# Optimization experiments

Hardware: AMD Instinct MI355X
Metric: run time of the kernel (lower is better)

## Reference

```python
import jax, jax.numpy as jnp
import numpy as np

MU_P = 0.15
MASK_ID = 103
VOCAB = 30522


def setup_inputs() -> dict:
    key = jax.random.key(0)
    k1, k2 = jax.random.split(key)
    B, C, S = 1024, 4, 2048
    # first half = per-token sampling weights, second half = shared_tokens (unused by the math)
    my_attention_mask = jax.random.uniform(k1, (B, C, 2 * S), dtype=jnp.float32)
    attention_mask = jnp.ones((B, C, S), dtype=jnp.int32)  # tokenizer attention mask
    input_ids = jax.random.randint(k2, (B, C, S), 0, VOCAB, dtype=jnp.int32)
    return {"my_attention_mask": my_attention_mask,
            "attention_mask": attention_mask,
            "input_ids": input_ids}


def reference(my_attention_mask, attention_mask, input_ids):
    """Weighted sampling WITHOUT replacement per (batch, choice) row via Gumbel-top-k.

    Original loops over (k, j), draws num_to_mask = floor(sum(tok_mask) * N(mu_p, sigma))
    indices from the nonzero weights in my_attention_mask[..., :S] (prob ~ weight),
    masks those token positions in input_ids and emits the indicator mask.
    Gumbel-top-k: keys = log(w) + Gumbel noise; the top-num_to_mask keys are a
    weighted sample without replacement from w. Zero-weight positions get -inf keys.
    """
    B, C, S = input_ids.shape
    w = my_attention_mask[..., :S]  # [B, C, S] sampling weights

    key = jax.random.key(42)
    kg, kn = jax.random.split(key)
    sigma = min(0.05, MU_P / 4.0)
    frac = MU_P + sigma * jax.random.normal(kn, (B, C), dtype=jnp.float32)
    num_to_mask = jnp.floor(
        attention_mask.sum(axis=-1).astype(jnp.float32) * frac
    ).astype(jnp.int32)  # [B, C]

    log_w = jnp.where(w > 0, jnp.log(jnp.maximum(w, 1e-30)), -jnp.inf)
    keys = log_w + jax.random.gumbel(kg, w.shape, dtype=jnp.float32)  # [B, C, S]

    # rank[i] = position of i in descending key order (double argsort)
    order = jnp.argsort(-keys, axis=-1)
    rank = jnp.argsort(order, axis=-1)
    new_attention_mask = (rank < num_to_mask[..., None]).astype(jnp.int32)  # [B, C, S]

    new_input_ids = jnp.where(new_attention_mask == 1, MASK_ID, input_ids)
    discriminator_labels = -new_attention_mask
    return new_input_ids, new_attention_mask, discriminator_labels
```

## Files before the change

### kernel.cpp

```cpp
#include <hip/hip_runtime.h>
#include <stdint.h>
#include <math.h>

#define SLEN 2048
#define EPT 8
#define NTHREADS 256
#define TOKENS_PER_OUT 8388608

__host__ __device__ __forceinline__ void tf2x32(uint32_t k0, uint32_t k1,
                                                uint32_t x0, uint32_t x1,
                                                uint32_t &o0, uint32_t &o1) {
  uint32_t ks2 = 0x1BD11BDAu ^ k0 ^ k1;
  x0 += k0; x1 += k1;
#define TFR(r) { x0 += x1; x1 = (x1 << (r)) | (x1 >> (32 - (r))); x1 ^= x0; }
  TFR(13) TFR(15) TFR(26) TFR(6)
  x0 += k1;  x1 += ks2 + 1u;
  TFR(17) TFR(29) TFR(16) TFR(24)
  x0 += ks2; x1 += k0 + 2u;
  TFR(13) TFR(15) TFR(26) TFR(6)
  x0 += k0;  x1 += k1 + 3u;
  TFR(17) TFR(29) TFR(16) TFR(24)
  x0 += k1;  x1 += ks2 + 4u;
  TFR(13) TFR(15) TFR(26) TFR(6)
  x0 += ks2; x1 += k0 + 5u;
#undef TFR
  o0 = x0; o1 = x1;
}

__device__ __forceinline__ void tf4_bits(uint32_t k0, uint32_t k1,
                                         uint32_t cbase, uint32_t bits[4]) {
  const uint32_t ks2 = 0x1BD11BDAu ^ k0 ^ k1;
  uint32_t x0[4], x1[4];
#pragma unroll
  for (int i = 0; i < 4; ++i) { x0[i] = k0; x1[i] = (cbase + (uint32_t)i) + k1; }
#define TFR4(r)                                                         \
  _Pragma("unroll")                                                     \
  for (int i = 0; i < 4; ++i) {                                         \
    x0[i] += x1[i];                                                     \
    x1[i] = (x1[i] << (r)) | (x1[i] >> (32 - (r)));                     \
    x1[i] ^= x0[i];                                                     \
  }
#define INJ4(a, b)                                                      \
  _Pragma("unroll")                                                     \
  for (int i = 0; i < 4; ++i) { x0[i] += (a); x1[i] += (b); }
  TFR4(13) TFR4(15) TFR4(26) TFR4(6)
  INJ4(k1, ks2 + 1u)
  TFR4(17) TFR4(29) TFR4(16) TFR4(24)
  INJ4(ks2, k0 + 2u)
  TFR4(13) TFR4(15) TFR4(26) TFR4(6)
  INJ4(k0, k1 + 3u)
  TFR4(17) TFR4(29) TFR4(16) TFR4(24)
  INJ4(k1, ks2 + 4u)
  TFR4(13) TFR4(15) TFR4(26) TFR4(6)
  INJ4(ks2, k0 + 5u)
#undef TFR4
#undef INJ4
#pragma unroll
  for (int i = 0; i < 4; ++i) bits[i] = x0[i] ^ x1[i];
}

__device__ __forceinline__ float u01_from_bits(uint32_t bits) {
  return __uint_as_float((bits >> 9) | 0x3F800000u) - 1.0f;
}

__device__ __forceinline__ void log4_cr(const float x[4], float out[4]) {
#pragma clang fp contract(off)
  double m[4]; int e[4];
#pragma unroll
  for (int i = 0; i < 4; ++i) {
    long long b = __double_as_longlong((double)x[i]);
    e[i] = (int)(b >> 52) - 1023;
    m[i] = __longlong_as_double((b & 0x000FFFFFFFFFFFFFLL) | 0x3FF0000000000000LL);
  }
#pragma unroll
  for (int i = 0; i < 4; ++i) {
    bool c = m[i] > 1.4142135623730951;
    m[i] = c ? 0.5 * m[i] : m[i];
    e[i] += c ? 1 : 0;
  }
  double mp1[4], y[4];
#pragma unroll
  for (int i = 0; i < 4; ++i) mp1[i] = m[i] + 1.0;
#pragma unroll
  for (int i = 0; i < 4; ++i) y[i] = __builtin_amdgcn_rcp(mp1[i]);
#pragma unroll
  for (int i = 0; i < 4; ++i) y[i] = fma(fma(-mp1[i], y[i], 1.0), y[i], y[i]);
  double r[4], t[4], p[4];
#pragma unroll
  for (int i = 0; i < 4; ++i) r[i] = (m[i] - 1.0) * y[i];
#pragma unroll
  for (int i = 0; i < 4; ++i) t[i] = r[i] * r[i];
#pragma unroll
  for (int i = 0; i < 4; ++i) p[i] = fma(0.07692307692307693, t[i], 0.09090909090909091);
#pragma unroll
  for (int i = 0; i < 4; ++i) p[i] = fma(p[i], t[i], 0.1111111111111111);
#pragma unroll
  for (int i = 0; i < 4; ++i) p[i] = fma(p[i], t[i], 0.14285714285714285);
#pragma unroll
  for (int i = 0; i < 4; ++i) p[i] = fma(p[i], t[i], 0.2);
#pragma unroll
  for (int i = 0; i < 4; ++i) p[i] = fma(p[i], t[i], 0.3333333333333333);
#pragma unroll
  for (int i = 0; i < 4; ++i) p[i] = fma(p[i], t[i], 1.0);
#pragma unroll
  for (int i = 0; i < 4; ++i)
    out[i] = (float)fma((double)e[i], 0.6931471805599453, 2.0 * (r[i] * p[i]));
}

__device__ __forceinline__ float log_cr(float x) {
  float in[4] = {x, x, x, x}, o[4];
  log4_cr(in, o);
  return o[0];
}

__device__ float erfinv_xla(float x) {
#pragma clang fp contract(off)
  float x2  = x * x;
  float nx2 = -x2;
  float l1p;
  if (fabsf(nx2) < 1e-4f) {
    l1p = (-0.5f * nx2 + 1.0f) * nx2;
  } else {
    l1p = log_cr(1.0f + nx2);
  }
  float w = -l1p;
  float p;
  if (w < 5.0f) {
    float ww = w - 2.5f;
    p = 2.81022636e-08f;
    p = p * ww + 3.43273939e-07f;
    p = p * ww + -3.5233877e-06f;
    p = p * ww + -4.39150654e-06f;
    p = p * ww + 0.00021858087f;
    p = p * ww + -0.00125372503f;
    p = p * ww + -0.00417768164f;
    p = p * ww + 0.246640727f;
    p = p * ww + 1.50140941f;
  } else {
    float ww = sqrtf(w) - 3.0f;
    p = -0.000200214257f;
    p = p * ww + 0.000100950558f;
    p = p * ww + 0.00134934322f;
    p = p * ww + -0.00367342844f;
    p = p * ww + 0.00573950773f;
    p = p * ww + -0.0076224613f;
    p = p * ww + 0.00943887047f;
    p = p * ww + 1.00167406f;
    p = p * ww + 2.83297682f;
  }
  return p * x;
}

__global__ __launch_bounds__(NTHREADS, 6)
void gumbel_topk_mask(const float* __restrict__ wfull,
                      const int*   __restrict__ attn,
                      const int*   __restrict__ ids,
                      int* __restrict__ out,
                      uint32_t kg0, uint32_t kg1, uint32_t kn0, uint32_t kn1) {
#pragma clang fp contract(off)
  const int row  = blockIdx.x;
  const int t    = threadIdx.x;
  const int lane = t & 63;
  const int wid  = t >> 6;

  __shared__ __align__(16) uint32_t hist[2][256];
  __shared__ uint32_t wsum[4];
  __shared__ uint32_t prefix_s;
  __shared__ uint32_t remaining_s;
  __shared__ int      done_s;

  const size_t rbase = (size_t)row * SLEN;
  const size_t wbase = (size_t)row * (2 * SLEN);
  const int    base  = t * EPT;

  hist[0][t] = 0u;
  hist[1][t] = 0u;

  const float4* wv4 = (const float4*)(wfull + wbase + base);
  float4 w0 = wv4[0], w1 = wv4[1];
  const int4* av4 = (const int4*)(attn + rbase + base);
  int4 a0 = av4[0], a1 = av4[1];
  const int4* iv4 = (const int4*)(ids + rbase + base);
  int4 i0 = iv4[0], i1 = iv4[1];
  int psum = a0.x + a0.y + a0.z + a0.w + a1.x + a1.y + a1.z + a1.w;

  float wl[EPT] = {w0.x, w0.y, w0.z, w0.w, w1.x, w1.y, w1.z, w1.w};
  uint32_t mloc[EPT];
#pragma unroll
  for (int g = 0; g < 2; ++g) {
    uint32_t bits[4];
    tf4_bits(kg0, kg1, (uint32_t)(rbase + base + 4 * g), bits);
    float uu[4];
#pragma unroll
    for (int j = 0; j < 4; ++j) {
      float f = u01_from_bits(bits[j]);
      uu[j] = fmaxf(1.17549435e-38f, f * 1.0f + 1.17549435e-38f);
    }
    float l1[4];
    log4_cr(uu, l1);
    float wm[4];
#pragma unroll
    for (int j = 0; j < 4; ++j) wm[j] = fmaxf(wl[4 * g + j], 1e-30f);
    float lw[4];
    log4_cr(wm, lw);
    float nl1[4];
#pragma unroll
    for (int j = 0; j < 4; ++j) nl1[j] = -l1[j];
    float l2[4];
    log4_cr(nl1, l2);
#pragma unroll
    for (int j = 0; j < 4; ++j) {
      float key = (wl[4 * g + j] > 0.0f) ? (lw[j] + (-l2[j])) : -__builtin_inff();
      uint32_t kb = __float_as_uint(key);
      uint32_t mv = (kb & 0x80000000u) ? ~kb : (kb | 0x80000000u);
      mloc[4 * g + j] = mv;
    }
  }

#pragma unroll
  for (int off = 32; off; off >>= 1) psum += __shfl_down(psum, off, 64);
  if (lane == 0) wsum[wid] = (uint32_t)psum;
  if (t == 0) { prefix_s = 0u; done_s = 0; }
  __syncthreads();

#pragma unroll
  for (int e = 0; e < EPT; ++e) atomicAdd(&hist[0][mloc[e] >> 24], 1u);

  int cur = 0;
  for (int p = 3; p >= 0; --p) {
    __syncthreads();
    if (t < 64) {
      uint32_t need = 0u;
      if (p == 3) {
        int asum = (int)(wsum[0] + wsum[1] + wsum[2] + wsum[3]);
        uint32_t o0, o1;
        tf2x32(kn0, kn1, 0u, (uint32_t)row, o0, o1);
        float f   = u01_from_bits(o0 ^ o1);
        float lo  = __uint_as_float(0xBF7FFFFFu);
        float u2  = fmaxf(lo, f * 2.0f + lo);
        float z   = erfinv_xla(u2);
        float nrm = 1.4142135623730951f * z;
        float frac = 0.15f + 0.0375f * nrm;
        int kk = (int)floorf((float)asum * frac);
        if (kk <= 0)         { if (t == 0) { prefix_s = 0xFFFFFFFFu; remaining_s = 0u;   done_s = 1; } }
        else if (kk >= SLEN) { if (t == 0) { prefix_s = 0u;          remaining_s = SLEN; done_s = 1; } }
        else need = (uint32_t)kk;
      } else {
        need = remaining_s;
      }
      if (need) {
        uint4 hq = ((const uint4*)hist[cur])[t];
        uint32_t gs  = hq.x + hq.y + hq.z + hq.w;
        uint32_t sfx = gs;
#pragma unroll
        for (int off = 1; off < 64; off <<= 1) {
          uint32_t n = __shfl_down(sfx, off, 64);
          if (t + off < 64) sfx += n;
        }
        uint32_t Gex = sfx - gs;
        uint32_t S3 = Gex;
        uint32_t S2 = S3 + hq.w;
        uint32_t S1 = S2 + hq.z;
        uint32_t S0 = S1 + hq.y;
        uint32_t hh[4] = {hq.x, hq.y, hq.z, hq.w};
        uint32_t SS[4] = {S0, S1, S2, S3};
#pragma unroll
        for (int i = 0; i < 4; ++i) {
          if (hh[i] && SS[i] < need && need <= SS[i] + hh[i]) {
            prefix_s |= ((uint32_t)(4 * t + i)) << (8 * p);
            uint32_t rem = need - SS[i];
            remaining_s = rem;
            if (rem == hh[i]) done_s = 1;
          }
        }
      }
    } else {
      int idx = t - 64;
      hist[cur ^ 1][idx] = 0u;
      if (idx < 64) hist[cur ^ 1][idx + 192] = 0u;
    }
    __syncthreads();
    if (done_s) break;
    if (p > 0) {
      uint32_t pref = prefix_s;
      int sh = 8 * p;
#pragma unroll
      for (int e = 0; e < EPT; ++e) {
        uint32_t m = mloc[e];
        if ((m >> sh) == (pref >> sh))
          atomicAdd(&hist[cur ^ 1][(m >> (sh - 8)) & 255u], 1u);
      }
    }
    cur ^= 1;
  }
  uint32_t T = prefix_s;
  uint32_t r = remaining_s;

  int local_eq = 0;
#pragma unroll
  for (int e = 0; e < EPT; ++e) local_eq += (mloc[e] == T) ? 1 : 0;
  uint32_t v = (uint32_t)local_eq;
#pragma unroll
  for (int off = 1; off < 64; off <<= 1) {
    uint32_t n = __shfl_up(v, off, 64);
    if (lane >= off) v += n;
  }
  if (lane == 63) wsum[wid] = v;
  __syncthreads();
  uint32_t add = 0;
  for (int i = 0; i < wid; ++i) add += wsum[i];
  uint32_t excl = add + v - (uint32_t)local_eq;

  int idv[EPT] = {i0.x, i0.y, i0.z, i0.w, i1.x, i1.y, i1.z, i1.w};
  int oid[EPT], omk[EPT], olb[EPT];
#pragma unroll
  for (int e = 0; e < EPT; ++e) {
    uint32_t m = mloc[e];
    bool eq  = (m == T);
    bool msk = (m > T) || (eq && (excl < r));
    excl += eq ? 1u : 0u;
    oid[e] = msk ? 103 : idv[e];
    omk[e] = msk ? 1 : 0;
    olb[e] = msk ? -1 : 0;
  }
  int4* po = (int4*)(out + rbase + base);
  po[0] = make_int4(oid[0], oid[1], oid[2], oid[3]);
  po[1] = make_int4(oid[4], oid[5], oid[6], oid[7]);
  int4* pm = (int4*)(out + TOKENS_PER_OUT + rbase + base);
  pm[0] = make_int4(omk[0], omk[1], omk[2], omk[3]);
  pm[1] = make_int4(omk[4], omk[5], omk[6], omk[7]);
  int4* pl = (int4*)(out + 2 * TOKENS_PER_OUT + rbase + base);
  pl[0] = make_int4(olb[0], olb[1], olb[2], olb[3]);
  pl[1] = make_int4(olb[4], olb[5], olb[6], olb[7]);
}

extern "C" void kernel_launch(void* const* d_in, const int* in_sizes, int n_in,
                              void* d_out, int out_size, void* d_ws, size_t ws_size,
                              hipStream_t stream) {
  (void)n_in; (void)d_ws; (void)ws_size; (void)out_size;
  const float* wfull = (const float*)d_in[0];
  const int*   attn  = (const int*)d_in[1];
  const int*   ids   = (const int*)d_in[2];
  int* out = (int*)d_out;

  uint32_t kg0, kg1, kn0, kn1, o0, o1;
  tf2x32(0u, 42u, 0u, 0u, o0, o1); kg0 = o0; kg1 = o1;
  tf2x32(0u, 42u, 0u, 1u, o0, o1); kn0 = o0; kn1 = o1;

  int rows = in_sizes[1] / SLEN;
  hipLaunchKernelGGL(gumbel_topk_mask, dim3(rows), dim3(NTHREADS), 0, stream,
                     wfull, attn, ids, out, kg0, kg1, kn0, kn1);
}
```

Baseline: 207.5 us.

## Batch logs 8-wide with sched barriers and integer-based mantissa extraction

Widens the double-precision log routine from 4 to 8 lanes and puts scheduling barriers between each polynomial stage, so independent FP64 ops interleave and hide latency. Mantissa/exponent extraction now uses 32-bit integer ops on the float bits instead of a float-to-double conversion. The scalar log also loses its wasted 4-wide evaluation. Launch bounds drop from 6 to 5 blocks per CU to allow more registers, which risks lower occupancy and latency hiding.

```diff
diff --git a/kernel.cpp b/kernel.cpp
--- a/kernel.cpp
+++ b/kernel.cpp
@@ -39,7 +39,8 @@
     x0[i] += x1[i];                                                     \
     x1[i] = (x1[i] << (r)) | (x1[i] >> (32 - (r)));                     \
     x1[i] ^= x0[i];                                                     \
-  }
+  }                                                                     \
+  __builtin_amdgcn_sched_barrier(0);
 #define INJ4(a, b)                                                      \
   _Pragma("unroll")                                                     \
   for (int i = 0; i < 4; ++i) { x0[i] += (a); x1[i] += (b); }
@@ -63,54 +64,93 @@
   return __uint_as_float((bits >> 9) | 0x3F800000u) - 1.0f;
 }
 
-__device__ __forceinline__ void log4_cr(const float x[4], float out[4]) {
+#define SBAR() __builtin_amdgcn_sched_barrier(0)
+
+__device__ __forceinline__ void log8_cr(const float x[8], float out[8]) {
 #pragma clang fp contract(off)
-  double m[4]; int e[4];
-#pragma unroll
-  for (int i = 0; i < 4; ++i) {
-    long long b = __double_as_longlong((double)x[i]);
-    e[i] = (int)(b >> 52) - 1023;
-    m[i] = __longlong_as_double((b & 0x000FFFFFFFFFFFFFLL) | 0x3FF0000000000000LL);
-  }
-#pragma unroll
-  for (int i = 0; i < 4; ++i) {
-    bool c = m[i] > 1.4142135623730951;
-    m[i] = c ? 0.5 * m[i] : m[i];
-    e[i] += c ? 1 : 0;
-  }
-  double mp1[4], y[4];
-#pragma unroll
-  for (int i = 0; i < 4; ++i) mp1[i] = m[i] + 1.0;
-#pragma unroll
-  for (int i = 0; i < 4; ++i) y[i] = __builtin_amdgcn_rcp(mp1[i]);
-#pragma unroll
-  for (int i = 0; i < 4; ++i) y[i] = fma(fma(-mp1[i], y[i], 1.0), y[i], y[i]);
-  double r[4], t[4], p[4];
-#pragma unroll
-  for (int i = 0; i < 4; ++i) r[i] = (m[i] - 1.0) * y[i];
-#pragma unroll
-  for (int i = 0; i < 4; ++i) t[i] = r[i] * r[i];
-#pragma unroll
-  for (int i = 0; i < 4; ++i) p[i] = fma(0.07692307692307693, t[i], 0.09090909090909091);
-#pragma unroll
-  for (int i = 0; i < 4; ++i) p[i] = fma(p[i], t[i], 0.1111111111111111);
-#pragma unroll
-  for (int i = 0; i < 4; ++i) p[i] = fma(p[i], t[i], 0.14285714285714285);
-#pragma unroll
-  for (int i = 0; i < 4; ++i) p[i] = fma(p[i], t[i], 0.2);
-#pragma unroll
-  for (int i = 0; i < 4; ++i) p[i] = fma(p[i], t[i], 0.3333333333333333);
-#pragma unroll
-  for (int i = 0; i < 4; ++i) p[i] = fma(p[i], t[i], 1.0);
-#pragma unroll
-  for (int i = 0; i < 4; ++i)
-    out[i] = (float)fma((double)e[i], 0.6931471805599453, 2.0 * (r[i] * p[i]));
+  double m[8]; int e[8];
+#pragma unroll
+  for (int i = 0; i < 8; ++i) {
+    uint32_t xb   = __float_as_uint(x[i]);
+    uint32_t mant = xb & 0x7FFFFFu;
+    int      ee   = (int)(xb >> 23) - 127;
+    bool     big  = mant > 0x3504F3u;
+    e[i] = ee + (big ? 1 : 0);
+    uint32_t hi = (big ? 0x3FE00000u : 0x3FF00000u) | (mant >> 3);
+    uint32_t lo = mant << 29;
+    m[i] = __longlong_as_double(((long long)hi << 32) | (long long)lo);
+  }
+  SBAR();
+  double mp1[8];
+#pragma unroll
+  for (int i = 0; i < 8; ++i) mp1[i] = m[i] + 1.0;
+  SBAR();
+  double y[8];
+#pragma unroll
+  for (int i = 0; i < 8; ++i) y[i] = __builtin_amdgcn_rcp(mp1[i]);
+  SBAR();
+#pragma unroll
+  for (int i = 0; i < 8; ++i) y[i] = fma(fma(-mp1[i], y[i], 1.0), y[i], y[i]);
+  SBAR();
+  double r[8];
+#pragma unroll
+  for (int i = 0; i < 8; ++i) r[i] = (m[i] - 1.0) * y[i];
+  SBAR();
+  double t[8];
+#pragma unroll
+  for (int i = 0; i < 8; ++i) t[i] = r[i] * r[i];
+  SBAR();
+  double p[8];
+#pragma unroll
+  for (int i = 0; i < 8; ++i) p[i] = fma(0.07692307692307693, t[i], 0.09090909090909091);
+  SBAR();
+#pragma unroll
+  for (int i = 0; i < 8; ++i) p[i] = fma(p[i], t[i], 0.1111111111111111);
+  SBAR();
+#pragma unroll
+  for (int i = 0; i < 8; ++i) p[i] = fma(p[i], t[i], 0.14285714285714285);
+  SBAR();
+#pragma unroll
+  for (int i = 0; i < 8; ++i) p[i] = fma(p[i], t[i], 0.2);
+  SBAR();
+#pragma unroll
+  for (int i = 0; i < 8; ++i) p[i] = fma(p[i], t[i], 0.3333333333333333);
+  SBAR();
+#pragma unroll
+  for (int i = 0; i < 8; ++i) p[i] = fma(p[i], t[i], 1.0);
+  SBAR();
+#pragma unroll
+  for (int i = 0; i < 8; ++i) r[i] = r[i] + r[i];
+  SBAR();
+#pragma unroll
+  for (int i = 0; i < 8; ++i) p[i] = r[i] * p[i];
+  SBAR();
+#pragma unroll
+  for (int i = 0; i < 8; ++i)
+    out[i] = (float)fma((double)e[i], 0.6931471805599453, p[i]);
 }
 
 __device__ __forceinline__ float log_cr(float x) {
-  float in[4] = {x, x, x, x}, o[4];
-  log4_cr(in, o);
-  return o[0];
+#pragma clang fp contract(off)
+  uint32_t xb   = __float_as_uint(x);
+  uint32_t mant = xb & 0x7FFFFFu;
+  int      e    = (int)(xb >> 23) - 127;
+  bool     big  = mant > 0x3504F3u;
+  e += big ? 1 : 0;
+  uint32_t hi = (big ? 0x3FE00000u : 0x3FF00000u) | (mant >> 3);
+  double m = __longlong_as_double(((long long)hi << 32) | (long long)(mant << 29));
+  double mp1 = m + 1.0;
+  double y = __builtin_amdgcn_rcp(mp1);
+  y = fma(fma(-mp1, y, 1.0), y, y);
+  double r = (m - 1.0) * y;
+  double t = r * r;
+  double p = fma(0.07692307692307693, t, 0.09090909090909091);
+  p = fma(p, t, 0.1111111111111111);
+  p = fma(p, t, 0.14285714285714285);
+  p = fma(p, t, 0.2);
+  p = fma(p, t, 0.3333333333333333);
+  p = fma(p, t, 1.0);
+  return (float)fma((double)e, 0.6931471805599453, (r + r) * p);
 }
 
 __device__ float erfinv_xla(float x) {
@@ -151,7 +191,7 @@
   return p * x;
 }
 
-__global__ __launch_bounds__(NTHREADS, 6)
+__global__ __launch_bounds__(NTHREADS, 5)
 void gumbel_topk_mask(const float* __restrict__ wfull,
                       const int*   __restrict__ attn,
                       const int*   __restrict__ ids,
@@ -180,42 +220,44 @@
   float4 w0 = wv4[0], w1 = wv4[1];
   const int4* av4 = (const int4*)(attn + rbase + base);
   int4 a0 = av4[0], a1 = av4[1];
+  int psum = a0.x + a0.y + a0.z + a0.w + a1.x + a1.y + a1.z + a1.w;
+
+  uint32_t bits[EPT];
+  tf4_bits(kg0, kg1, (uint32_t)(rbase + base + 0), bits + 0);
+  tf4_bits(kg0, kg1, (uint32_t)(rbase + base + 4), bits + 4);
+  SBAR();
+
+  float wl[EPT] = {w0.x, w0.y, w0.z, w0.w, w1.x, w1.y, w1.z, w1.w};
+  float uu[EPT];
+#pragma unroll
+  for (int e = 0; e < EPT; ++e) {
+    float f = u01_from_bits(bits[e]);
+    uu[e] = fmaxf(1.17549435e-38f, f * 1.0f + 1.17549435e-38f);
+  }
+  SBAR();
+  float l1[EPT];
+  log8_cr(uu, l1);
+  float wm[EPT];
+#pragma unroll
+  for (int e = 0; e < EPT; ++e) wm[e] = fmaxf(wl[e], 1e-30f);
+  float lw[EPT];
+  log8_cr(wm, lw);
+  float nl1[EPT];
+#pragma unroll
+  for (int e = 0; e < EPT; ++e) nl1[e] = -l1[e];
+  float l2[EPT];
+  log8_cr(nl1, l2);
+  SBAR();
+  uint32_t mloc[EPT];
+#pragma unroll
+  for (int e = 0; e < EPT; ++e) {
+    float key = (wl[e] > 0.0f) ? (lw[e] + (-l2[e])) : -__builtin_inff();
+    uint32_t kb = __float_as_uint(key);
+    mloc[e] = (kb & 0x80000000u) ? ~kb : (kb | 0x80000000u);
+  }
+
   const int4* iv4 = (const int4*)(ids + rbase + base);
   int4 i0 = iv4[0], i1 = iv4[1];
-  int psum = a0.x + a0.y + a0.z + a0.w + a1.x + a1.y + a1.z + a1.w;
-
-  float wl[EPT] = {w0.x, w0.y, w0.z, w0.w, w1.x, w1.y, w1.z, w1.w};
-  uint32_t mloc[EPT];
-#pragma unroll
-  for (int g = 0; g < 2; ++g) {
-    uint32_t bits[4];
-    tf4_bits(kg0, kg1, (uint32_t)(rbase + base + 4 * g), bits);
-    float uu[4];
-#pragma unroll
-    for (int j = 0; j < 4; ++j) {
-      float f = u01_from_bits(bits[j]);
-      uu[j] = fmaxf(1.17549435e-38f, f * 1.0f + 1.17549435e-38f);
-    }
-    float l1[4];
-    log4_cr(uu, l1);
-    float wm[4];
-#pragma unroll
-    for (int j = 0; j < 4; ++j) wm[j] = fmaxf(wl[4 * g + j], 1e-30f);
-    float lw[4];
-    log4_cr(wm, lw);
-    float nl1[4];
-#pragma unroll
-    for (int j = 0; j < 4; ++j) nl1[j] = -l1[j];
-    float l2[4];
-    log4_cr(nl1, l2);
-#pragma unroll
-    for (int j = 0; j < 4; ++j) {
-      float key = (wl[4 * g + j] > 0.0f) ? (lw[j] + (-l2[j])) : -__builtin_inff();
-      uint32_t kb = __float_as_uint(key);
-      uint32_t mv = (kb & 0x80000000u) ? ~kb : (kb | 0x80000000u);
-      mloc[4 * g + j] = mv;
-    }
-  }
 
 #pragma unroll
   for (int off = 32; off; off >>= 1) psum += __shfl_down(psum, off, 64);
```

Result: faster. 202.3 us (-2.5%).
